# Optimization experiments

Hardware: AMD Instinct MI355X
Metric: run time of the kernel (lower is better)

Reference implementation:

```python
import jax, jax.numpy as jnp
import numpy as np

N, D, H, E_RAW = 100000, 128, 8, 1600000
C = D // H  # head dim = 16
NEG_SLOPE = 0.2
LN_EPS = 1e-5


def _glorot(key, shape):
    fan_in, fan_out = shape[0], shape[-1]
    lim = (6.0 / (fan_in + fan_out)) ** 0.5
    return jax.random.uniform(key, shape, jnp.float32, -lim, lim)


def setup_inputs() -> dict:
    key = jax.random.key(0)
    ks = jax.random.split(key, 16)
    inp = {
        "x": jax.random.normal(ks[0], (N, D), jnp.float32),
        "edge_index": jax.random.randint(ks[1], (2, E_RAW), 0, N, jnp.int64),
    }
    for l in range(2):
        o = 2 + 4 * l
        inp[f"Wl{l}"] = _glorot(ks[o + 0], (D, H * C))
        inp[f"Wr{l}"] = _glorot(ks[o + 1], (D, H * C))
        inp[f"att{l}"] = _glorot(ks[o + 2], (H, C))
        inp[f"b{l}"] = jnp.zeros((H * C,), jnp.float32)
        inp[f"g{l}"] = jnp.ones((D,), jnp.float32)
        inp[f"beta{l}"] = jnp.zeros((D,), jnp.float32)
    return inp


def _gatv2_layer(x, src, dst, Wl, Wr, att, b):
    # GATv2Conv: e_ij = att . leaky_relu(Wl x_j + Wr x_i); softmax over j -> i
    xl = (x @ Wl).reshape(N, H, C)  # source transform
    xr = (x @ Wr).reshape(N, H, C)  # target transform
    m = jax.nn.leaky_relu(xl[src] + xr[dst], NEG_SLOPE)  # [E,H,C]
    e = jnp.einsum("ehc,hc->eh", m, att)  # [E,H]
    emax = jax.ops.segment_max(e, dst, num_segments=N)[dst]
    ex = jnp.exp(e - emax)
    denom = jax.ops.segment_sum(ex, dst, num_segments=N)[dst]
    alpha = ex / denom  # per-destination softmax
    out = jax.ops.segment_sum(xl[src] * alpha[:, :, None], dst, num_segments=N)
    return out.reshape(N, H * C) + b


def _layernorm(x, g, beta):
    mu = jnp.mean(x, axis=-1, keepdims=True)
    var = jnp.var(x, axis=-1, keepdims=True)
    return (x - mu) * jax.lax.rsqrt(var + LN_EPS) * g + beta


def reference(x, edge_index, Wl0, Wr0, att0, b0, g0, beta0,
              Wl1, Wr1, att1, b1, g1, beta1):
    # add_self_loops=True (PyG default): every node attends to itself
    loop = jnp.arange(N, dtype=edge_index.dtype)
    src = jnp.concatenate([edge_index[0], loop])
    dst = jnp.concatenate([edge_index[1], loop])
    params = [(Wl0, Wr0, att0, b0, g0, beta0), (Wl1, Wr1, att1, b1, g1, beta1)]
    for Wl, Wr, att, b, g, beta in params:
        residual = x
        h = _gatv2_layer(x, src, dst, Wl, Wr, att, b)  # dropout is identity (eval)
        h = jax.nn.elu(h)
        x = _layernorm(h + residual, g, beta)
    return x
```

## Files before the change

### kernel.cpp

```cpp
#include <hip/hip_runtime.h>
#include <cstdint>

#define LEAKY 0.2f
#define LN_EPS 1e-5f

typedef __attribute__((ext_vector_type(8))) short short8;
typedef __attribute__((ext_vector_type(4))) float f32x4;
typedef __attribute__((ext_vector_type(2))) float f32x2;

__device__ __forceinline__ ushort bf16_rne(float x) {
    unsigned u = __float_as_uint(x);
    unsigned r = (u + 0x7fffu + ((u >> 16) & 1u)) >> 16;
    return (ushort)r;
}
__device__ __forceinline__ float bf16_to_f(ushort h) {
    return __uint_as_float(((unsigned)h) << 16);
}
__device__ __forceinline__ f32x2 unpk(uint u) {
    f32x2 r;
    r.x = __uint_as_float(u << 16);
    r.y = __uint_as_float(u & 0xffff0000u);
    return r;
}

__global__ void hist_part(const int* __restrict__ ei, int er, int etot, int n,
                          int* __restrict__ deg) {
    const int xcd = blockIdx.x & 7;
    const int lo = (int)((long long)n * xcd >> 3);
    const int hi = (int)((long long)n * (xcd + 1) >> 3);
    const int stride = (gridDim.x >> 3) * blockDim.x;
    for (int e = (blockIdx.x >> 3) * blockDim.x + threadIdx.x; e < etot;
         e += stride) {
        int dst = (e < er) ? ei[er + e] : (e - er);
        if (dst >= lo && dst < hi) atomicAdd(&deg[dst], 1);
    }
}

__global__ void fill_part(const int* __restrict__ ei, int er, int etot, int n,
                          int* __restrict__ woff, int* __restrict__ colv) {
    const int xcd = blockIdx.x & 7;
    const int lo = (int)((long long)n * xcd >> 3);
    const int hi = (int)((long long)n * (xcd + 1) >> 3);
    const int stride = (gridDim.x >> 3) * blockDim.x;
    for (int e = (blockIdx.x >> 3) * blockDim.x + threadIdx.x; e < etot;
         e += stride) {
        int dst = (e < er) ? ei[er + e] : (e - er);
        if (dst >= lo && dst < hi) {
            int src = (e < er) ? ei[e] : dst;
            int pos = atomicAdd(&woff[dst], 1);
            colv[pos] = src;
        }
    }
}

__global__ __launch_bounds__(1024) void scanA(const int* __restrict__ deg,
                                              int* __restrict__ escan,
                                              int* __restrict__ bsum, int n) {
    __shared__ int wsum[16], wpre[16];
    const int lane = threadIdx.x & 63, wv = threadIdx.x >> 6;
    const int i = blockIdx.x * 1024 + threadIdx.x;
    int v = (i < n) ? deg[i] : 0;
    int x = v;
#pragma unroll
    for (int off = 1; off < 64; off <<= 1) {
        int y = __shfl_up(x, off, 64);
        if (lane >= off) x += y;
    }
    if (lane == 63) wsum[wv] = x;
    __syncthreads();
    if (wv == 0) {
        int s = (lane < 16) ? wsum[lane] : 0;
#pragma unroll
        for (int off = 1; off < 16; off <<= 1) {
            int y = __shfl_up(s, off, 64);
            if (lane >= off) s += y;
        }
        if (lane < 16) wpre[lane] = s;
    }
    __syncthreads();
    int excl = x - v + (wv ? wpre[wv - 1] : 0);
    if (i < n) escan[i] = excl;
    if (threadIdx.x == 1023) bsum[blockIdx.x] = wpre[15];
}

__global__ __launch_bounds__(1024) void scanB(const int* __restrict__ bsum,
                                              int* __restrict__ bpre, int nb,
                                              int* __restrict__ offs, int n) {
    __shared__ int wsum[16], wpre[16];
    const int lane = threadIdx.x & 63, wv = threadIdx.x >> 6;
    const int i = threadIdx.x;
    int v = (i < nb) ? bsum[i] : 0;
    int x = v;
#pragma unroll
    for (int off = 1; off < 64; off <<= 1) {
        int y = __shfl_up(x, off, 64);
        if (lane >= off) x += y;
    }
    if (lane == 63) wsum[wv] = x;
    __syncthreads();
    if (wv == 0) {
        int s = (lane < 16) ? wsum[lane] : 0;
#pragma unroll
        for (int off = 1; off < 16; off <<= 1) {
            int y = __shfl_up(s, off, 64);
            if (lane >= off) s += y;
        }
        if (lane < 16) wpre[lane] = s;
    }
    __syncthreads();
    if (i < nb) bpre[i] = x - v + (wv ? wpre[wv - 1] : 0);
    if (threadIdx.x == 1023) offs[n] = wpre[15];
}

__global__ void scanC(const int* __restrict__ escan, const int* __restrict__ bpre,
                      int* __restrict__ offs, int* __restrict__ woff, int n) {
    int i = blockIdx.x * 256 + threadIdx.x;
    if (i >= n) return;
    int o = escan[i] + bpre[i >> 10];
    offs[i] = o;
    woff[i] = o;
}

__global__ void cvt_w2(const float* __restrict__ Wl0, const float* __restrict__ Wr0,
                       const float* __restrict__ Wl1, const float* __restrict__ Wr1,
                       ushort* __restrict__ Whi, ushort* __restrict__ Wlo) {
    int t = blockIdx.x * 256 + threadIdx.x;
    int layer = t >> 15;
    int i = t & 32767;
    int colblk = i >> 11;
    int ks = (i >> 9) & 3;
    int lane = (i >> 3) & 63;
    int j = i & 7;
    int col = colblk * 16 + (lane & 15);
    int k = ks * 32 + (lane >> 4) * 8 + j;
    const float* Wl = layer ? Wl1 : Wl0;
    const float* Wr = layer ? Wr1 : Wr0;
    float v = (col < 128) ? Wl[(size_t)k * 128 + col]
                          : Wr[(size_t)k * 128 + (col - 128)];
    ushort h = bf16_rne(v);
    Whi[t] = h;
    Wlo[t] = bf16_rne(v - bf16_to_f(h));
}

template <bool ABF16>
__global__ __launch_bounds__(256) void gemm_mfma(
    const void* __restrict__ Xin,
    const ushort* __restrict__ Wfhi, const ushort* __restrict__ Wflo,
    uint* __restrict__ Olb, uint* __restrict__ Orb, int nrows) {
    __shared__ float4 xs[64 * 32];
    const int t = threadIdx.x;
    const int wave = t >> 6, lane = t & 63;
    const int m0 = blockIdx.x * 64;
    if (ABF16) {
        const uint4* Xv = (const uint4*)Xin + (size_t)m0 * 16;
        uint4* xsb = (uint4*)xs;
#pragma unroll
        for (int i = 0; i < 4; ++i) {
            int idx = i * 256 + t;
            int row = idx >> 4, kc = idx & 15;
            uint4 v = {0u, 0u, 0u, 0u};
            if (m0 + row < nrows) v = Xv[idx];
            xsb[row * 16 + (kc ^ (row & 7))] = v;
        }
    } else {
        const float4* Xv = (const float4*)Xin + (size_t)m0 * 32;
#pragma unroll
        for (int i = 0; i < 8; ++i) {
            int idx = i * 256 + t;
            int row = idx >> 5, kc = idx & 31;
            float4 v = {0.f, 0.f, 0.f, 0.f};
            if (m0 + row < nrows) v = Xv[idx];
            xs[row * 32 + (kc ^ (row & 7))] = v;
        }
    }
    __syncthreads();

    const int lrow = lane & 15;
    const int lkc = (lane >> 4) * 2;
    f32x4 acc[4][4];
#pragma unroll
    for (int mt = 0; mt < 4; ++mt)
#pragma unroll
        for (int nt = 0; nt < 4; ++nt) acc[mt][nt] = (f32x4){0.f, 0.f, 0.f, 0.f};

#pragma unroll 1
    for (int ks = 0; ks < 4; ++ks) {
        short8 ahi[4], alo[4];
#pragma unroll
        for (int mt = 0; mt < 4; ++mt) {
            const int row = mt * 16 + lrow;
            if (ABF16) {
                const int slot = ks * 4 + (lane >> 4);
                uint4 w = ((const uint4*)xs)[row * 16 + (slot ^ (row & 7))];
                ahi[mt] = *(const short8*)&w;
            } else {
                const int kc0 = ks * 8 + lkc;
                float4 v0 = xs[row * 32 + (kc0 ^ (row & 7))];
                float4 v1 = xs[row * 32 + ((kc0 + 1) ^ (row & 7))];
                float e[8];
                e[0] = v0.x; e[1] = v0.y; e[2] = v0.z; e[3] = v0.w;
                e[4] = v1.x; e[5] = v1.y; e[6] = v1.z; e[7] = v1.w;
#pragma unroll
                for (int j = 0; j < 8; ++j) {
                    ushort h = (ushort)(__float_as_uint(e[j]) >> 16);
                    ahi[mt][j] = (short)h;
                    alo[mt][j] = (short)bf16_rne(e[j] - bf16_to_f(h));
                }
            }
        }
#pragma unroll
        for (int nt = 0; nt < 4; ++nt) {
            size_t off = (((size_t)(wave * 4 + nt) * 4 + ks) * 64 + lane) * 8;
            short8 bhi = *(const short8*)&Wfhi[off];
            short8 blo = *(const short8*)&Wflo[off];
#pragma unroll
            for (int mt = 0; mt < 4; ++mt) {
                if (!ABF16)
                    acc[mt][nt] = __builtin_amdgcn_mfma_f32_16x16x32_bf16(
                        alo[mt], bhi, acc[mt][nt], 0, 0, 0);
                acc[mt][nt] = __builtin_amdgcn_mfma_f32_16x16x32_bf16(
                    ahi[mt], blo, acc[mt][nt], 0, 0, 0);
                acc[mt][nt] = __builtin_amdgcn_mfma_f32_16x16x32_bf16(
                    ahi[mt], bhi, acc[mt][nt], 0, 0, 0);
            }
        }
    }
    uint* __restrict__ O = (wave < 2) ? Olb : Orb;
    const int cbase = (wave * 64) & 127;
    const int crow0 = (lane >> 4) * 4;
    const bool evn = (lane & 1) == 0;
#pragma unroll
    for (int mt = 0; mt < 4; ++mt) {
#pragma unroll
        for (int i = 0; i < 4; ++i) {
            const int row = m0 + mt * 16 + crow0 + i;
#pragma unroll
            for (int nt = 0; nt < 4; ++nt) {
                float val = acc[mt][nt][i];
                float pv = __shfl_xor(val, 1);
                uint pk = (uint)bf16_rne(val) | ((uint)bf16_rne(pv) << 16);
                if (evn && row < nrows) {
                    const int col = cbase + nt * 16 + lrow;
                    O[(size_t)row * 64 + (col >> 1)] = pk;
                }
            }
        }
    }
}

template <bool RBF16, bool OBF16>
__global__ __launch_bounds__(256) void gat_agg(
    const uint* __restrict__ xl, const uint* __restrict__ xr,
    const int* __restrict__ offs, const int* __restrict__ colv,
    const float* __restrict__ att,
    const float* __restrict__ bias, const float* __restrict__ gamma,
    const float* __restrict__ beta, const void* __restrict__ resid,
    void* __restrict__ out, int nnode) {
    const int lane = threadIdx.x & 63;
    const int wid = __builtin_amdgcn_readfirstlane(threadIdx.x >> 6);
    const int wave0 = blockIdx.x * 4 + wid;
    const int wstride = gridDim.x * 4;
    const f32x2 att2 = ((const f32x2*)att)[lane];
    const f32x2 b2 = ((const f32x2*)bias)[lane];
    const f32x2 g2 = ((const f32x2*)gamma)[lane];
    const f32x2 be2 = ((const f32x2*)beta)[lane];
    for (int gid = wave0; gid < nnode; gid += wstride) {
        const uint xru = __builtin_nontemporal_load(xr + (size_t)gid * 64 + lane);
        const f32x2 xr2 = unpk(xru);
        float den = 0.f;
        f32x2 acc = {0.f, 0.f};
        int e = offs[gid];
        const int e1 = offs[gid + 1];
        for (; e + 4 <= e1; e += 4) {
            int s0 = __builtin_amdgcn_readfirstlane(colv[e]);
            int s1 = __builtin_amdgcn_readfirstlane(colv[e + 1]);
            int s2 = __builtin_amdgcn_readfirstlane(colv[e + 2]);
            int s3 = __builtin_amdgcn_readfirstlane(colv[e + 3]);
            uint u0 = xl[(size_t)s0 * 64 + lane];
            uint u1 = xl[(size_t)s1 * 64 + lane];
            uint u2 = xl[(size_t)s2 * 64 + lane];
            uint u3 = xl[(size_t)s3 * 64 + lane];
            f32x2 a0 = unpk(u0), a1 = unpk(u1), a2 = unpk(u2), a3 = unpk(u3);
            f32x2 m0 = a0 + xr2, m1 = a1 + xr2, m2 = a2 + xr2, m3 = a3 + xr2;
            f32x2 l0 = m0 * LEAKY, l1 = m1 * LEAKY, l2 = m2 * LEAKY, l3 = m3 * LEAKY;
            m0.x = fmaxf(m0.x, l0.x); m0.y = fmaxf(m0.y, l0.y);
            m1.x = fmaxf(m1.x, l1.x); m1.y = fmaxf(m1.y, l1.y);
            m2.x = fmaxf(m2.x, l2.x); m2.y = fmaxf(m2.y, l2.y);
            m3.x = fmaxf(m3.x, l3.x); m3.y = fmaxf(m3.y, l3.y);
            f32x2 t0 = m0 * att2, t1 = m1 * att2, t2 = m2 * att2, t3 = m3 * att2;
            float p0 = t0.x + t0.y, p1 = t1.x + t1.y;
            float p2 = t2.x + t2.y, p3 = t3.x + t3.y;
            p0 += __shfl_xor(p0, 1); p0 += __shfl_xor(p0, 2); p0 += __shfl_xor(p0, 4);
            p1 += __shfl_xor(p1, 1); p1 += __shfl_xor(p1, 2); p1 += __shfl_xor(p1, 4);
            p2 += __shfl_xor(p2, 1); p2 += __shfl_xor(p2, 2); p2 += __shfl_xor(p2, 4);
            p3 += __shfl_xor(p3, 1); p3 += __shfl_xor(p3, 2); p3 += __shfl_xor(p3, 4);
            float ex0 = __expf(p0), ex1 = __expf(p1);
            float ex2 = __expf(p2), ex3 = __expf(p3);
            den += (ex0 + ex1) + (ex2 + ex3);
            acc += a0 * ex0;
            acc += a1 * ex1;
            acc += a2 * ex2;
            acc += a3 * ex3;
        }
        for (; e < e1; ++e) {
            int s0 = __builtin_amdgcn_readfirstlane(colv[e]);
            uint u0 = xl[(size_t)s0 * 64 + lane];
            f32x2 a0 = unpk(u0);
            f32x2 m0 = a0 + xr2;
            f32x2 l0 = m0 * LEAKY;
            m0.x = fmaxf(m0.x, l0.x); m0.y = fmaxf(m0.y, l0.y);
            f32x2 t0 = m0 * att2;
            float p0 = t0.x + t0.y;
            p0 += __shfl_xor(p0, 1); p0 += __shfl_xor(p0, 2); p0 += __shfl_xor(p0, 4);
            float ex0 = __expf(p0);
            den += ex0;
            acc += a0 * ex0;
        }
        const float inv_den = 1.f / den;
        f32x2 v = acc * inv_den + b2;
        v.x = v.x > 0.f ? v.x : expm1f(v.x);
        v.y = v.y > 0.f ? v.y : expm1f(v.y);
        f32x2 r2;
        if (RBF16) {
            uint ru = __builtin_nontemporal_load(
                (const uint*)resid + (size_t)gid * 64 + lane);
            r2 = unpk(ru);
        } else {
            r2 = __builtin_nontemporal_load(
                (const f32x2*)resid + (size_t)gid * 64 + lane);
        }
        f32x2 tv = v + r2;
        float s = tv.x + tv.y, ss = tv.x * tv.x + tv.y * tv.y;
#pragma unroll
        for (int m = 1; m < 64; m <<= 1) {
            s += __shfl_xor(s, m);
            ss += __shfl_xor(ss, m);
        }
        const float mu = s * 0.0078125f;
        const float var = ss * 0.0078125f - mu * mu;
        const float iv = rsqrtf(var + LN_EPS);
        f32x2 o = (tv - mu) * iv * g2 + be2;
        if (OBF16) {
            uint po = (uint)bf16_rne(o.x) | ((uint)bf16_rne(o.y) << 16);
            __builtin_nontemporal_store(po, (uint*)out + (size_t)gid * 64 + lane);
        } else {
            __builtin_nontemporal_store(o, (f32x2*)out + (size_t)gid * 64 + lane);
        }
    }
}

extern "C" void kernel_launch(void* const* d_in, const int* in_sizes, int n_in,
                              void* d_out, int out_size, void* d_ws, size_t ws_size,
                              hipStream_t stream) {
    const float* x   = (const float*)d_in[0];
    const int*   ei  = (const int*)d_in[1];
    const float* Wl0 = (const float*)d_in[2];
    const float* Wr0 = (const float*)d_in[3];
    const float* at0 = (const float*)d_in[4];
    const float* b0  = (const float*)d_in[5];
    const float* g0  = (const float*)d_in[6];
    const float* be0 = (const float*)d_in[7];
    const float* Wl1 = (const float*)d_in[8];
    const float* Wr1 = (const float*)d_in[9];
    const float* at1 = (const float*)d_in[10];
    const float* b1  = (const float*)d_in[11];
    const float* g1  = (const float*)d_in[12];
    const float* be1 = (const float*)d_in[13];

    const int NF = in_sizes[0];
    const int n  = NF / 128;
    const int er = in_sizes[1] / 2;
    const int etot = er + n;
    const int nb = (n + 1023) / 1024;

    uint* A     = (uint*)d_ws;
    uint* B     = A + (size_t)NF / 2;
    uint* C1    = B + (size_t)NF / 2;
    ushort* Whi = (ushort*)(C1 + (size_t)NF / 2);
    ushort* Wlo = Whi + 65536;
    int* deg    = (int*)(Wlo + 65536);
    int* woff   = deg + n;
    int* offs   = woff + n;
    int* escan  = offs + (n + 4);
    int* bsum   = escan + n;
    int* bpre   = bsum + 1024;
    int* colv   = bpre + 1024;
    float* C    = (float*)d_out;

    (void)hipMemsetAsync(deg, 0, (size_t)n * sizeof(int), stream);
    hist_part<<<2048, 256, 0, stream>>>(ei, er, etot, n, deg);
    scanA<<<nb, 1024, 0, stream>>>(deg, escan, bsum, n);
    scanB<<<1, 1024, 0, stream>>>(bsum, bpre, nb, offs, n);
    scanC<<<(n + 255) / 256, 256, 0, stream>>>(escan, bpre, offs, woff, n);
    fill_part<<<2048, 256, 0, stream>>>(ei, er, etot, n, woff, colv);
    cvt_w2<<<256, 256, 0, stream>>>(Wl0, Wr0, Wl1, Wr1, Whi, Wlo);

    const int gblk = (n + 63) / 64;

    gemm_mfma<false><<<gblk, 256, 0, stream>>>(x, Whi, Wlo, A, B, n);
    gat_agg<false, true><<<2048, 256, 0, stream>>>(
        A, B, offs, colv, at0, b0, g0, be0, x, C1, n);
    gemm_mfma<true><<<gblk, 256, 0, stream>>>(C1, Whi + 32768, Wlo + 32768,
                                              A, B, n);
    gat_agg<true, false><<<2048, 256, 0, stream>>>(
        A, B, offs, colv, at1, b1, g1, be1, C1, C, n);
}
```

Baseline: 445.4 us.

## Process two destination nodes per wave with half-wave gathers of 4 channels

The aggregation kernel now assigns two destination nodes to each wave, with each 32-lane half handling one node and loading 8-byte (4 bf16 channel) chunks per lane instead of 4-byte chunks. Edge loops run to the larger of the two degrees, using clamped indices and masked exponentials, so the scalar tail loop is gone and head reductions need fewer shuffles. This is meant to raise gather width and latency hiding per wave. In exchange, per-edge source indices are now vector loads instead of readfirstlane scalars, and lanes waste work when the paired degrees differ.

```diff
diff --git a/kernel.cpp b/kernel.cpp
--- a/kernel.cpp
+++ b/kernel.cpp
@@ -7,6 +7,7 @@
 typedef __attribute__((ext_vector_type(8))) short short8;
 typedef __attribute__((ext_vector_type(4))) float f32x4;
 typedef __attribute__((ext_vector_type(2))) float f32x2;
+typedef __attribute__((ext_vector_type(2))) uint u32x2;
 
 __device__ __forceinline__ ushort bf16_rne(float x) {
     unsigned u = __float_as_uint(x);
@@ -16,10 +17,12 @@
 __device__ __forceinline__ float bf16_to_f(ushort h) {
     return __uint_as_float(((unsigned)h) << 16);
 }
-__device__ __forceinline__ f32x2 unpk(uint u) {
-    f32x2 r;
-    r.x = __uint_as_float(u << 16);
-    r.y = __uint_as_float(u & 0xffff0000u);
+__device__ __forceinline__ f32x4 unpk4(u32x2 u) {
+    f32x4 r;
+    r.x = __uint_as_float(u.x << 16);
+    r.y = __uint_as_float(u.x & 0xffff0000u);
+    r.z = __uint_as_float(u.y << 16);
+    r.w = __uint_as_float(u.y & 0xffff0000u);
     return r;
 }
 
@@ -257,94 +260,108 @@
     const float* __restrict__ beta, const void* __restrict__ resid,
     void* __restrict__ out, int nnode) {
     const int lane = threadIdx.x & 63;
-    const int wid = __builtin_amdgcn_readfirstlane(threadIdx.x >> 6);
-    const int wave0 = blockIdx.x * 4 + wid;
+    const int hl = lane & 31;
+    const int half = lane >> 5;
+    const int wave0 = blockIdx.x * 4 + (threadIdx.x >> 6);
     const int wstride = gridDim.x * 4;
-    const f32x2 att2 = ((const f32x2*)att)[lane];
-    const f32x2 b2 = ((const f32x2*)bias)[lane];
-    const f32x2 g2 = ((const f32x2*)gamma)[lane];
-    const f32x2 be2 = ((const f32x2*)beta)[lane];
-    for (int gid = wave0; gid < nnode; gid += wstride) {
-        const uint xru = __builtin_nontemporal_load(xr + (size_t)gid * 64 + lane);
-        const f32x2 xr2 = unpk(xru);
+    const int npair = (nnode + 1) >> 1;
+    const f32x4 att4 = ((const f32x4*)att)[hl];
+    const f32x4 b4 = ((const f32x4*)bias)[hl];
+    const f32x4 g4 = ((const f32x4*)gamma)[hl];
+    const f32x4 be4 = ((const f32x4*)beta)[hl];
+    const u32x2* __restrict__ xl2 = (const u32x2*)xl;
+    for (int p = wave0; p < npair; p += wstride) {
+        const int node = p * 2 + half;
+        const int nodec = node < nnode ? node : nnode - 1;
+        const u32x2 xru = __builtin_nontemporal_load(
+            (const u32x2*)xr + (size_t)nodec * 32 + hl);
+        const f32x4 xr4 = unpk4(xru);
         float den = 0.f;
-        f32x2 acc = {0.f, 0.f};
-        int e = offs[gid];
-        const int e1 = offs[gid + 1];
-        for (; e + 4 <= e1; e += 4) {
-            int s0 = __builtin_amdgcn_readfirstlane(colv[e]);
-            int s1 = __builtin_amdgcn_readfirstlane(colv[e + 1]);
-            int s2 = __builtin_amdgcn_readfirstlane(colv[e + 2]);
-            int s3 = __builtin_amdgcn_readfirstlane(colv[e + 3]);
-            uint u0 = xl[(size_t)s0 * 64 + lane];
-            uint u1 = xl[(size_t)s1 * 64 + lane];
-            uint u2 = xl[(size_t)s2 * 64 + lane];
-            uint u3 = xl[(size_t)s3 * 64 + lane];
-            f32x2 a0 = unpk(u0), a1 = unpk(u1), a2 = unpk(u2), a3 = unpk(u3);
-            f32x2 m0 = a0 + xr2, m1 = a1 + xr2, m2 = a2 + xr2, m3 = a3 + xr2;
-            f32x2 l0 = m0 * LEAKY, l1 = m1 * LEAKY, l2 = m2 * LEAKY, l3 = m3 * LEAKY;
+        f32x4 acc = {0.f, 0.f, 0.f, 0.f};
+        int e = offs[nodec];
+        const int e1 = offs[nodec + 1];
+        const int e1m = e1 - 1;
+        int deg = e1 - e;
+        int mdeg = max(deg, __shfl_xor(deg, 32));
+        int niter = (mdeg + 3) >> 2;
+        for (int it = 0; it < niter; ++it) {
+            int ek0 = min(e, e1m), ek1 = min(e + 1, e1m);
+            int ek2 = min(e + 2, e1m), ek3 = min(e + 3, e1m);
+            int s0 = colv[ek0], s1 = colv[ek1], s2 = colv[ek2], s3 = colv[ek3];
+            u32x2 u0 = xl2[(size_t)s0 * 32 + hl];
+            u32x2 u1 = xl2[(size_t)s1 * 32 + hl];
+            u32x2 u2 = xl2[(size_t)s2 * 32 + hl];
+            u32x2 u3 = xl2[(size_t)s3 * 32 + hl];
+            f32x4 a0 = unpk4(u0), a1 = unpk4(u1), a2 = unpk4(u2), a3 = unpk4(u3);
+            f32x4 m0 = a0 + xr4, m1 = a1 + xr4, m2 = a2 + xr4, m3 = a3 + xr4;
+            f32x4 l0 = m0 * LEAKY, l1 = m1 * LEAKY;
+            f32x4 l2 = m2 * LEAKY, l3 = m3 * LEAKY;
             m0.x = fmaxf(m0.x, l0.x); m0.y = fmaxf(m0.y, l0.y);
+            m0.z = fmaxf(m0.z, l0.z); m0.w = fmaxf(m0.w, l0.w);
             m1.x = fmaxf(m1.x, l1.x); m1.y = fmaxf(m1.y, l1.y);
+            m1.z = fmaxf(m1.z, l1.z); m1.w = fmaxf(m1.w, l1.w);
             m2.x = fmaxf(m2.x, l2.x); m2.y = fmaxf(m2.y, l2.y);
+            m2.z = fmaxf(m2.z, l2.z); m2.w = fmaxf(m2.w, l2.w);
             m3.x = fmaxf(m3.x, l3.x); m3.y = fmaxf(m3.y, l3.y);
-            f32x2 t0 = m0 * att2, t1 = m1 * att2, t2 = m2 * att2, t3 = m3 * att2;
-            float p0 = t0.x + t0.y, p1 = t1.x + t1.y;
-            float p2 = t2.x + t2.y, p3 = t3.x + t3.y;
-            p0 += __shfl_xor(p0, 1); p0 += __shfl_xor(p0, 2); p0 += __shfl_xor(p0, 4);
-            p1 += __shfl_xor(p1, 1); p1 += __shfl_xor(p1, 2); p1 += __shfl_xor(p1, 4);
-            p2 += __shfl_xor(p2, 1); p2 += __shfl_xor(p2, 2); p2 += __shfl_xor(p2, 4);
-            p3 += __shfl_xor(p3, 1); p3 += __shfl_xor(p3, 2); p3 += __shfl_xor(p3, 4);
-            float ex0 = __expf(p0), ex1 = __expf(p1);
-            float ex2 = __expf(p2), ex3 = __expf(p3);
+            m3.z = fmaxf(m3.z, l3.z); m3.w = fmaxf(m3.w, l3.w);
+            f32x4 t0 = m0 * att4, t1 = m1 * att4, t2 = m2 * att4, t3 = m3 * att4;
+            float p0 = (t0.x + t0.y) + (t0.z + t0.w);
+            float p1 = (t1.x + t1.y) + (t1.z + t1.w);
+            float p2 = (t2.x + t2.y) + (t2.z + t2.w);
+            float p3 = (t3.x + t3.y) + (t3.z + t3.w);
+            p0 += __shfl_xor(p0, 1); p0 += __shfl_xor(p0, 2);
+            p1 += __shfl_xor(p1, 1); p1 += __shfl_xor(p1, 2);
+            p2 += __shfl_xor(p2, 1); p2 += __shfl_xor(p2, 2);
+            p3 += __shfl_xor(p3, 1); p3 += __shfl_xor(p3, 2);
+            float ex0 = (e < e1) ? __expf(p0) : 0.f;
+            float ex1 = (e + 1 < e1) ? __expf(p1) : 0.f;
+            float ex2 = (e + 2 < e1) ? __expf(p2) : 0.f;
+            float ex3 = (e + 3 < e1) ? __expf(p3) : 0.f;
             den += (ex0 + ex1) + (ex2 + ex3);
             acc += a0 * ex0;
             acc += a1 * ex1;
             acc += a2 * ex2;
             acc += a3 * ex3;
-        }
-        for (; e < e1; ++e) {
-            int s0 = __builtin_amdgcn_readfirstlane(colv[e]);
-            uint u0 = xl[(size_t)s0 * 64 + lane];
-            f32x2 a0 = unpk(u0);
-            f32x2 m0 = a0 + xr2;
-            f32x2 l0 = m0 * LEAKY;
-            m0.x = fmaxf(m0.x, l0.x); m0.y = fmaxf(m0.y, l0.y);
-            f32x2 t0 = m0 * att2;
-            float p0 = t0.x + t0.y;
-            p0 += __shfl_xor(p0, 1); p0 += __shfl_xor(p0, 2); p0 += __shfl_xor(p0, 4);
-            float ex0 = __expf(p0);
-            den += ex0;
-            acc += a0 * ex0;
+            e += 4;
         }
         const float inv_den = 1.f / den;
-        f32x2 v = acc * inv_den + b2;
+        f32x4 v = acc * inv_den + b4;
         v.x = v.x > 0.f ? v.x : expm1f(v.x);
         v.y = v.y > 0.f ? v.y : expm1f(v.y);
-        f32x2 r2;
+        v.z = v.z > 0.f ? v.z : expm1f(v.z);
+        v.w = v.w > 0.f ? v.w : expm1f(v.w);
+        f32x4 r4;
         if (RBF16) {
-            uint ru = __builtin_nontemporal_load(
-                (const uint*)resid + (size_t)gid * 64 + lane);
-            r2 = unpk(ru);
+            u32x2 ru = __builtin_nontemporal_load(
+                (const u32x2*)resid + (size_t)nodec * 32 + hl);
+            r4 = unpk4(ru);
         } else {
-            r2 = __builtin_nontemporal_load(
-                (const f32x2*)resid + (size_t)gid * 64 + lane);
-        }
-        f32x2 tv = v + r2;
-        float s = tv.x + tv.y, ss = tv.x * tv.x + tv.y * tv.y;
-#pragma unroll
-        for (int m = 1; m < 64; m <<= 1) {
+            r4 = __builtin_nontemporal_load(
+                (const f32x4*)resid + (size_t)nodec * 32 + hl);
+        }
+        f32x4 tv = v + r4;
+        float s = (tv.x + tv.y) + (tv.z + tv.w);
+        float ss = (tv.x * tv.x + tv.y * tv.y) + (tv.z * tv.z + tv.w * tv.w);
+#pragma unroll
+        for (int m = 1; m < 32; m <<= 1) {
             s += __shfl_xor(s, m);
             ss += __shfl_xor(ss, m);
         }
         const float mu = s * 0.0078125f;
         const float var = ss * 0.0078125f - mu * mu;
         const float iv = rsqrtf(var + LN_EPS);
-        f32x2 o = (tv - mu) * iv * g2 + be2;
-        if (OBF16) {
-            uint po = (uint)bf16_rne(o.x) | ((uint)bf16_rne(o.y) << 16);
-            __builtin_nontemporal_store(po, (uint*)out + (size_t)gid * 64 + lane);
-        } else {
-            __builtin_nontemporal_store(o, (f32x2*)out + (size_t)gid * 64 + lane);
+        f32x4 o = (tv - mu) * iv * g4 + be4;
+        if (node < nnode) {
+            if (OBF16) {
+                u32x2 po;
+                po.x = (uint)bf16_rne(o.x) | ((uint)bf16_rne(o.y) << 16);
+                po.y = (uint)bf16_rne(o.z) | ((uint)bf16_rne(o.w) << 16);
+                __builtin_nontemporal_store(
+                    po, (u32x2*)out + (size_t)node * 32 + hl);
+            } else {
+                __builtin_nontemporal_store(
+                    o, (f32x4*)out + (size_t)node * 32 + hl);
+            }
         }
     }
 }
```

Measured after the change: 480.6 us. 7.9% more time.
